# Kernel tuning notes

Measured on AMD Instinct MI355X. Metric: run time of the kernel, lower is better.

Reference implementation:

```python
import jax, jax.numpy as jnp
import numpy as np

B, S, H, C = 8, 4096, 768, 64

def setup_inputs() -> dict:
    key = jax.random.key(0)
    ks = jax.random.split(key, 13)
    s_h = 1.0 / np.sqrt(H)
    s_c = 1.0 / np.sqrt(C)
    return {
        "hidden_states": jax.random.normal(ks[0], (B, S, H), jnp.float32),
        "attention_mask": jnp.ones((B, S), jnp.int32),
        # contrast_transform: Linear(H, C)
        "W_ct": jax.random.uniform(ks[1], (H, C), jnp.float32, -s_h, s_h),
        "b_ct": jax.random.uniform(ks[2], (C,), jnp.float32, -s_h, s_h),
        # conflict_detector: Linear(C, 1)
        "W_cd": jax.random.uniform(ks[3], (C, 1), jnp.float32, -s_c, s_c),
        "b_cd": jax.random.uniform(ks[4], (1,), jnp.float32, -s_c, s_c),
        # expectation_mlp: Linear(H,C) -> ReLU -> Linear(C,1)
        "W_e1": jax.random.uniform(ks[5], (H, C), jnp.float32, -s_h, s_h),
        "b_e1": jax.random.uniform(ks[6], (C,), jnp.float32, -s_h, s_h),
        "W_e2": jax.random.uniform(ks[7], (C, 1), jnp.float32, -s_c, s_c),
        "b_e2": jax.random.uniform(ks[8], (1,), jnp.float32, -s_c, s_c),
        # surprise query/key: Linear(H, C)
        "W_q": jax.random.uniform(ks[9], (H, C), jnp.float32, -s_h, s_h),
        "b_q": jax.random.uniform(ks[10], (C,), jnp.float32, -s_h, s_h),
        "W_k": jax.random.uniform(ks[11], (H, C), jnp.float32, -s_h, s_h),
        "b_k": jax.random.uniform(ks[12], (C,), jnp.float32, -s_h, s_h),
    }

def reference(hidden_states, attention_mask, W_ct, b_ct, W_cd, b_cd,
              W_e1, b_e1, W_e2, b_e2, W_q, b_q, W_k, b_k):
    # semantic conflict: sigmoid(Linear1(Linear(h)))  -> (B, S)
    compressed = hidden_states @ W_ct + b_ct                      # (B,S,C)
    semantic_conflict = jax.nn.sigmoid((compressed @ W_cd + b_cd)[..., 0])
    # expectation violation: sigmoid(MLP(h)) -> (B, S)
    h1 = jax.nn.relu(hidden_states @ W_e1 + b_e1)                 # (B,S,C)
    expectation_violation = jax.nn.sigmoid((h1 @ W_e2 + b_e2)[..., 0])
    # contextual surprise: mean over keys of softmax(QK^T / sqrt(C))
    Q = hidden_states @ W_q + b_q                                 # (B,S,C)
    K = hidden_states @ W_k + b_k                                 # (B,S,C)
    scores = jnp.einsum('bqc,bkc->bqk', Q, K) / jnp.sqrt(jnp.float32(Q.shape[-1]))
    contextual_surprise = jnp.mean(jax.nn.softmax(scores, axis=-1), axis=-1)  # (B,S)
    return semantic_conflict, expectation_violation, contextual_surprise
```

## Files before the change

### kernel.cpp

```cpp
#include <hip/hip_runtime.h>
#include <hip/hip_bf16.h>
#include <math.h>

typedef __bf16 bf16;
typedef __bf16 bf16x8 __attribute__((ext_vector_type(8)));
typedef float  f32x4  __attribute__((ext_vector_type(4)));

static constexpr int kTokens = 32768;
static constexpr int kH   = 768;
static constexpr int kC   = 64;
static constexpr int kCK  = 64;
static constexpr int kNQ  = kH / kCK;
static constexpr int kTB  = 64;
static constexpr int kBW  = 72;

__global__ __launch_bounds__(256) void prep_kernel(
    const float* __restrict__ W_ct, const float* __restrict__ b_ct,
    const float* __restrict__ W_cd, const float* __restrict__ b_cd,
    const float* __restrict__ W_e1, bf16* __restrict__ Wt,
    float* __restrict__ bsc) {
    __shared__ float t[64][65];
    const int tid = threadIdx.x;
    const int b   = blockIdx.x;
    if (b < 12) {
        const int k0 = b * 64;
        #pragma unroll
        for (int i = 0; i < 16; ++i) {
            int idx = tid + i * 256;
            int k = idx >> 6, n = idx & 63;
            t[k][n] = W_e1[(size_t)(k0 + k) * kC + n];
        }
        __syncthreads();
        #pragma unroll
        for (int i = 0; i < 16; ++i) {
            int idx = tid + i * 256;
            int n = idx >> 6, k = idx & 63;
            Wt[(size_t)n * kH + k0 + k] = (bf16)t[k][n];
        }
    } else if (b < 24) {
        const int k0 = (b - 12) * 64;
        #pragma unroll
        for (int i = 0; i < 16; ++i) {
            int idx = tid + i * 256;
            int k = idx >> 6, c = idx & 63;
            t[k][c] = W_ct[(size_t)(k0 + k) * kC + c];
        }
        __syncthreads();
        if (tid < 64) {
            float s = 0.f;
            #pragma unroll
            for (int c = 0; c < kC; ++c) s += t[tid][c] * W_cd[c];
            Wt[(size_t)kC * kH + k0 + tid] = (bf16)s;
        }
    } else {
        if (tid < 64) {
            float v = b_ct[tid] * W_cd[tid];
            #pragma unroll
            for (int m = 1; m < 64; m <<= 1) v += __shfl_xor(v, m);
            if (tid == 0) bsc[0] = v + b_cd[0];
        }
    }
}

__device__ __forceinline__ void issue_a(const float* __restrict__ hs_blk, int q,
                                        float* __restrict__ buf, int wv, int lane) {
    #pragma unroll
    for (int r = 0; r < 4; ++r) {
        const int span   = wv * 4 + r;
        const int absrow = span * 4 + (lane >> 4);
        const int colB   = (lane & 15) * 16;
        const int scol   = colB ^ ((absrow & 7) << 4);
        const char* src  = (const char*)(hs_blk + (size_t)absrow * kH + q * kCK) + scol;
        float* dst = buf + span * 256;
        __builtin_amdgcn_global_load_lds(
            (const __attribute__((address_space(1))) void*)src,
            (__attribute__((address_space(3))) void*)dst, 16, 0, 0);
    }
}

__global__ __launch_bounds__(256, 3) void incong_main(
    const float* __restrict__ hs,
    const bf16*  __restrict__ Wt,
    const float* __restrict__ bsc_p,
    const float* __restrict__ b_e1,
    const float* __restrict__ W_e2,
    const float* __restrict__ b_e2,
    float* __restrict__ out)
{
    __shared__ float lds_a[2][kTB][kCK];
    __shared__ bf16  lds_w[65][kBW];

    const int tid  = threadIdx.x;
    const int lane = tid & 63;
    const int wv   = tid >> 6;
    const int r16  = lane & 15;
    const int kg   = lane >> 4;

    const int tok0 = blockIdx.x * kTB;
    const float* hs_blk = hs + (size_t)tok0 * kH;

    f32x4 acc[5];
    #pragma unroll
    for (int n = 0; n < 5; ++n) acc[n] = (f32x4){0.f, 0.f, 0.f, 0.f};

    const int      trow  = wv * 16 + r16;
    const unsigned sw    = (unsigned)((r16 & 7) << 4);
    const char*    ab0   = (const char*)&lds_a[0][trow][0];
    const char*    ab1   = (const char*)&lds_a[1][trow][0];

    issue_a(hs_blk, 0, &lds_a[0][0][0], wv, lane);

    for (int q = 0; q < kNQ; ++q) {
        const int b = q & 1;
        {
            const int c0 = tid, c1 = tid + 256;
            const int row0 = c0 >> 3, col0 = (c0 & 7) * 8;
            const int row1 = c1 >> 3, col1 = (c1 & 7) * 8;
            bf16x8 v0 = *reinterpret_cast<const bf16x8*>(&Wt[(size_t)row0 * kH + q * kCK + col0]);
            bf16x8 v1 = *reinterpret_cast<const bf16x8*>(&Wt[(size_t)row1 * kH + q * kCK + col1]);
            bf16x8 v2;
            if (tid < 8) v2 = *reinterpret_cast<const bf16x8*>(&Wt[(size_t)64 * kH + q * kCK + tid * 8]);
            if (q + 1 < kNQ) issue_a(hs_blk, q + 1, &lds_a[b ^ 1][0][0], wv, lane);
            *reinterpret_cast<bf16x8*>(&lds_w[row0][col0]) = v0;
            *reinterpret_cast<bf16x8*>(&lds_w[row1][col1]) = v1;
            if (tid < 8) *reinterpret_cast<bf16x8*>(&lds_w[64][tid * 8]) = v2;
        }
        asm volatile("s_waitcnt lgkmcnt(0)" ::: "memory");
        __builtin_amdgcn_s_barrier();
        asm volatile("" ::: "memory");

        const char* abase = b ? ab1 : ab0;
        #pragma unroll
        for (int s = 0; s < 2; ++s) {
            const unsigned o = (unsigned)(s * 128 + kg * 32);
            const f32x4 a0 = *reinterpret_cast<const f32x4*>(abase + (o ^ sw));
            const f32x4 a1 = *reinterpret_cast<const f32x4*>(abase + ((o + 16u) ^ sw));
            bf16x8 af;
            af[0] = (bf16)a0[0]; af[1] = (bf16)a0[1]; af[2] = (bf16)a0[2]; af[3] = (bf16)a0[3];
            af[4] = (bf16)a1[0]; af[5] = (bf16)a1[1]; af[6] = (bf16)a1[2]; af[7] = (bf16)a1[3];
            #pragma unroll
            for (int n = 0; n < 4; ++n) {
                const bf16x8 bfr = *reinterpret_cast<const bf16x8*>(
                    &lds_w[n * 16 + r16][s * 32 + kg * 8]);
                acc[n] = __builtin_amdgcn_mfma_f32_16x16x32_bf16(af, bfr, acc[n], 0, 0, 0);
            }
            {
                const bf16x8 b4 = *reinterpret_cast<const bf16x8*>(&lds_w[64][s * 32 + kg * 8]);
                acc[4] = __builtin_amdgcn_mfma_f32_16x16x32_bf16(af, b4, acc[4], 0, 0, 0);
            }
        }
        asm volatile("" ::: "memory");
        __builtin_amdgcn_s_barrier();
    }

    float part[4] = {0.f, 0.f, 0.f, 0.f};
    #pragma unroll
    for (int n = 0; n < 4; ++n) {
        const int cidx = n * 16 + r16;
        const float be = b_e1[cidx];
        const float we = W_e2[cidx];
        #pragma unroll
        for (int r = 0; r < 4; ++r)
            part[r] += fmaxf(acc[n][r] + be, 0.f) * we;
    }
    #pragma unroll
    for (int m = 1; m < 16; m <<= 1) {
        #pragma unroll
        for (int r = 0; r < 4; ++r) part[r] += __shfl_xor(part[r], m);
    }
    if (r16 == 0) {
        const float bsc = bsc_p[0];
        const float be2 = b_e2[0];
        #pragma unroll
        for (int r = 0; r < 4; ++r) {
            const int tok = tok0 + wv * 16 + kg * 4 + r;
            const float sc = acc[4][r] + bsc;
            out[tok]               = 1.f / (1.f + __expf(-sc));
            out[kTokens + tok]     = 1.f / (1.f + __expf(-(part[r] + be2)));
            out[2 * kTokens + tok] = 1.f / 4096.f;
        }
    }
}

extern "C" void kernel_launch(void* const* d_in, const int* in_sizes, int n_in,
                              void* d_out, int out_size, void* d_ws, size_t ws_size,
                              hipStream_t stream) {
    const float* hs   = (const float*)d_in[0];
    const float* W_ct = (const float*)d_in[2];
    const float* b_ct = (const float*)d_in[3];
    const float* W_cd = (const float*)d_in[4];
    const float* b_cd = (const float*)d_in[5];
    const float* W_e1 = (const float*)d_in[6];
    const float* b_e1 = (const float*)d_in[7];
    const float* W_e2 = (const float*)d_in[8];
    const float* b_e2 = (const float*)d_in[9];

    bf16*  Wt  = (bf16*)d_ws;
    float* bsc = (float*)((char*)d_ws + (size_t)80 * kH * sizeof(bf16));

    prep_kernel<<<25, 256, 0, stream>>>(W_ct, b_ct, W_cd, b_cd, W_e1, Wt, bsc);

    incong_main<<<kTokens / kTB, 256, 0, stream>>>(
        hs, Wt, bsc, b_e1, W_e2, b_e2, (float*)d_out);
}
```

Measured before the change: 27.69 us.

## Fuse weight prep into main kernel with global flag spin-wait

Folds the weight-transpose/fold prep kernel into the main GEMM kernel. The first 25 blocks act as producers and signal completion through an atomic counter, while every block spins on that counter after issuing its first activation tile load. This removes one kernel launch and lets the activation prefetch overlap with weight preparation. In exchange it adds a memset launch, a grid-wide spin wait that depends on the producer blocks being resident, extra LDS for the transpose tile, and lower occupancy (launch bounds 2 instead of 3).

```diff
diff --git a/kernel.cpp b/kernel.cpp
--- a/kernel.cpp
+++ b/kernel.cpp
@@ -13,54 +13,7 @@
 static constexpr int kNQ  = kH / kCK;
 static constexpr int kTB  = 64;
 static constexpr int kBW  = 72;
-
-__global__ __launch_bounds__(256) void prep_kernel(
-    const float* __restrict__ W_ct, const float* __restrict__ b_ct,
-    const float* __restrict__ W_cd, const float* __restrict__ b_cd,
-    const float* __restrict__ W_e1, bf16* __restrict__ Wt,
-    float* __restrict__ bsc) {
-    __shared__ float t[64][65];
-    const int tid = threadIdx.x;
-    const int b   = blockIdx.x;
-    if (b < 12) {
-        const int k0 = b * 64;
-        #pragma unroll
-        for (int i = 0; i < 16; ++i) {
-            int idx = tid + i * 256;
-            int k = idx >> 6, n = idx & 63;
-            t[k][n] = W_e1[(size_t)(k0 + k) * kC + n];
-        }
-        __syncthreads();
-        #pragma unroll
-        for (int i = 0; i < 16; ++i) {
-            int idx = tid + i * 256;
-            int n = idx >> 6, k = idx & 63;
-            Wt[(size_t)n * kH + k0 + k] = (bf16)t[k][n];
-        }
-    } else if (b < 24) {
-        const int k0 = (b - 12) * 64;
-        #pragma unroll
-        for (int i = 0; i < 16; ++i) {
-            int idx = tid + i * 256;
-            int k = idx >> 6, c = idx & 63;
-            t[k][c] = W_ct[(size_t)(k0 + k) * kC + c];
-        }
-        __syncthreads();
-        if (tid < 64) {
-            float s = 0.f;
-            #pragma unroll
-            for (int c = 0; c < kC; ++c) s += t[tid][c] * W_cd[c];
-            Wt[(size_t)kC * kH + k0 + tid] = (bf16)s;
-        }
-    } else {
-        if (tid < 64) {
-            float v = b_ct[tid] * W_cd[tid];
-            #pragma unroll
-            for (int m = 1; m < 64; m <<= 1) v += __shfl_xor(v, m);
-            if (tid == 0) bsc[0] = v + b_cd[0];
-        }
-    }
-}
+static constexpr unsigned kProducers = 25;
 
 __device__ __forceinline__ void issue_a(const float* __restrict__ hs_blk, int q,
                                         float* __restrict__ buf, int wv, int lane) {
@@ -78,26 +31,82 @@
     }
 }
 
-__global__ __launch_bounds__(256, 3) void incong_main(
+__global__ __launch_bounds__(256, 2) void incong_fused(
     const float* __restrict__ hs,
-    const bf16*  __restrict__ Wt,
-    const float* __restrict__ bsc_p,
-    const float* __restrict__ b_e1,
-    const float* __restrict__ W_e2,
-    const float* __restrict__ b_e2,
+    const float* __restrict__ W_ct, const float* __restrict__ b_ct,
+    const float* __restrict__ W_cd, const float* __restrict__ b_cd,
+    const float* __restrict__ W_e1, const float* __restrict__ b_e1,
+    const float* __restrict__ W_e2, const float* __restrict__ b_e2,
+    bf16* __restrict__ Wt,
+    float* __restrict__ bsc_p,
+    unsigned* __restrict__ flag,
     float* __restrict__ out)
 {
     __shared__ float lds_a[2][kTB][kCK];
     __shared__ bf16  lds_w[65][kBW];
+    __shared__ float t[64][65];
 
     const int tid  = threadIdx.x;
     const int lane = tid & 63;
     const int wv   = tid >> 6;
     const int r16  = lane & 15;
     const int kg   = lane >> 4;
-
-    const int tok0 = blockIdx.x * kTB;
+    const int b    = blockIdx.x;
+
+    const int tok0 = b * kTB;
     const float* hs_blk = hs + (size_t)tok0 * kH;
+
+    issue_a(hs_blk, 0, &lds_a[0][0][0], wv, lane);
+
+    if (b < 12) {
+        const int k0 = b * 64;
+        #pragma unroll
+        for (int i = 0; i < 16; ++i) {
+            int idx = tid + i * 256;
+            int k = idx >> 6, n = idx & 63;
+            t[k][n] = W_e1[(size_t)(k0 + k) * kC + n];
+        }
+        __syncthreads();
+        #pragma unroll
+        for (int i = 0; i < 16; ++i) {
+            int idx = tid + i * 256;
+            int n = idx >> 6, k = idx & 63;
+            Wt[(size_t)n * kH + k0 + k] = (bf16)t[k][n];
+        }
+    } else if (b < 24) {
+        const int k0 = (b - 12) * 64;
+        #pragma unroll
+        for (int i = 0; i < 16; ++i) {
+            int idx = tid + i * 256;
+            int k = idx >> 6, c = idx & 63;
+            t[k][c] = W_ct[(size_t)(k0 + k) * kC + c];
+        }
+        __syncthreads();
+        if (tid < 64) {
+            float s = 0.f;
+            #pragma unroll
+            for (int c = 0; c < kC; ++c) s += t[tid][c] * W_cd[c];
+            Wt[(size_t)kC * kH + k0 + tid] = (bf16)s;
+        }
+    } else if (b == 24) {
+        if (tid < 64) {
+            float v = b_ct[tid] * W_cd[tid];
+            #pragma unroll
+            for (int m = 1; m < 64; m <<= 1) v += __shfl_xor(v, m);
+            if (tid == 0) bsc_p[0] = v + b_cd[0];
+        }
+    }
+    if (b < kProducers) {
+        __threadfence();
+        __syncthreads();
+        if (tid == 0)
+            __hip_atomic_fetch_add(flag, 1u, __ATOMIC_RELEASE, __HIP_MEMORY_SCOPE_AGENT);
+    }
+    if (tid == 0) {
+        while (__hip_atomic_load(flag, __ATOMIC_ACQUIRE, __HIP_MEMORY_SCOPE_AGENT) < kProducers)
+            __builtin_amdgcn_s_sleep(2);
+    }
+    __syncthreads();
 
     f32x4 acc[5];
     #pragma unroll
@@ -108,10 +117,8 @@
     const char*    ab0   = (const char*)&lds_a[0][trow][0];
     const char*    ab1   = (const char*)&lds_a[1][trow][0];
 
-    issue_a(hs_blk, 0, &lds_a[0][0][0], wv, lane);
-
     for (int q = 0; q < kNQ; ++q) {
-        const int b = q & 1;
+        const int pb = q & 1;
         {
             const int c0 = tid, c1 = tid + 256;
             const int row0 = c0 >> 3, col0 = (c0 & 7) * 8;
@@ -120,7 +127,7 @@
             bf16x8 v1 = *reinterpret_cast<const bf16x8*>(&Wt[(size_t)row1 * kH + q * kCK + col1]);
             bf16x8 v2;
             if (tid < 8) v2 = *reinterpret_cast<const bf16x8*>(&Wt[(size_t)64 * kH + q * kCK + tid * 8]);
-            if (q + 1 < kNQ) issue_a(hs_blk, q + 1, &lds_a[b ^ 1][0][0], wv, lane);
+            if (q + 1 < kNQ) issue_a(hs_blk, q + 1, &lds_a[pb ^ 1][0][0], wv, lane);
             *reinterpret_cast<bf16x8*>(&lds_w[row0][col0]) = v0;
             *reinterpret_cast<bf16x8*>(&lds_w[row1][col1]) = v1;
             if (tid < 8) *reinterpret_cast<bf16x8*>(&lds_w[64][tid * 8]) = v2;
@@ -129,7 +136,7 @@
         __builtin_amdgcn_s_barrier();
         asm volatile("" ::: "memory");
 
-        const char* abase = b ? ab1 : ab0;
+        const char* abase = pb ? ab1 : ab0;
         #pragma unroll
         for (int s = 0; s < 2; ++s) {
             const unsigned o = (unsigned)(s * 128 + kg * 32);
@@ -195,11 +202,13 @@
     const float* W_e2 = (const float*)d_in[8];
     const float* b_e2 = (const float*)d_in[9];
 
-    bf16*  Wt  = (bf16*)d_ws;
-    float* bsc = (float*)((char*)d_ws + (size_t)80 * kH * sizeof(bf16));
-
-    prep_kernel<<<25, 256, 0, stream>>>(W_ct, b_ct, W_cd, b_cd, W_e1, Wt, bsc);
-
-    incong_main<<<kTokens / kTB, 256, 0, stream>>>(
-        hs, Wt, bsc, b_e1, W_e2, b_e2, (float*)d_out);
+    bf16*     Wt   = (bf16*)d_ws;
+    float*    bsc  = (float*)((char*)d_ws + (size_t)80 * kH * sizeof(bf16));
+    unsigned* flag = (unsigned*)((char*)d_ws + 256 * 1024);
+
+    hipMemsetAsync(flag, 0, sizeof(unsigned), stream);
+
+    incong_fused<<<kTokens / kTB, 256, 0, stream>>>(
+        hs, W_ct, b_ct, W_cd, b_cd, W_e1, b_e1, W_e2, b_e2,
+        Wt, bsc, flag, (float*)d_out);
 }
```

New measurement: 58.01 us. +109.5%, slower.
